# Optimization experiments

Measured on AMD Instinct MI355X. Metric: run time of the kernel, lower is better.

Reference implementation:

```python
import jax, jax.numpy as jnp
import numpy as np

B, TQ, TV, D, UNITS = 4, 256, 256, 512, 512
NEG_INF = -1e9

def setup_inputs() -> dict:
    key = jax.random.key(0)
    ks = jax.random.split(key, 5)
    return {
        "query": jax.random.normal(ks[0], (B, TQ, D), dtype=jnp.float32),
        "value": jax.random.normal(ks[1], (B, TV, D), dtype=jnp.float32),
        "mask": jnp.ones((B, TV), dtype=bool),
        "W1": jax.random.normal(ks[2], (D, UNITS), dtype=jnp.float32) * (1.0 / np.sqrt(D)),
        "W2": jax.random.normal(ks[3], (D, UNITS), dtype=jnp.float32) * (1.0 / np.sqrt(D)),
        "scale": jax.random.normal(ks[4], (UNITS,), dtype=jnp.float32),
    }

def reference(query, value, mask, W1, W2, scale):
    # Dual projections
    q = query @ W1                      # [B,Tq,U]
    k = value @ W2                      # [B,Tv,U]
    # Additive (Bahdanau) scores: sum(scale * tanh(q + k)) over units
    # broadcast tensor [B,Tq,Tv,U] is what the kernel would tile/fuse away
    t = jnp.tanh(q[:, :, None, :] + k[:, None, :, :])   # [B,Tq,Tv,U]
    scores = jnp.einsum('btvu,u->btv', t, scale)         # [B,Tq,Tv]
    # mask over value (key) positions
    scores = jnp.where(mask[:, None, :], scores, NEG_INF)
    attn = jax.nn.softmax(scores, axis=-1)               # [B,Tq,Tv]
    context = jnp.einsum('btv,bvd->btd', attn, value)    # [B,Tq,D]
    return context, attn
```

## Files before the change

### kernel.cpp

```cpp
#include <hip/hip_runtime.h>

typedef float f4 __attribute__((ext_vector_type(4)));
typedef float f2 __attribute__((ext_vector_type(2)));
typedef short short8 __attribute__((ext_vector_type(8)));
typedef float f32x4 __attribute__((ext_vector_type(4)));

#define NEG_INF -1e9f

__device__ inline void bsplit(float x, unsigned short& h, unsigned short& l) {
  union { float f; unsigned u; } a; a.f = x;
  unsigned rh = (a.u + 0x7fffu + ((a.u >> 16) & 1u)) >> 16;
  h = (unsigned short)rh;
  union { unsigned u; float f; } b; b.u = rh << 16;
  union { float f; unsigned u; } c; c.f = x - b.f;
  unsigned rl = (c.u + 0x7fffu + ((c.u >> 16) & 1u)) >> 16;
  l = (unsigned short)rl;
}

__device__ inline void gl_lds16(const void* g, void* l) {
  __builtin_amdgcn_global_load_lds(
      (const __attribute__((address_space(1))) unsigned int*)g,
      (__attribute__((address_space(3))) unsigned int*)l, 16, 0, 0);
}

__global__ __launch_bounds__(256) void conv_aw(
    const float* __restrict__ q, const float* __restrict__ v,
    const float* __restrict__ W1, const float* __restrict__ W2,
    unsigned short* __restrict__ Ahi, unsigned short* __restrict__ Alo,
    unsigned short* __restrict__ Whi, unsigned short* __restrict__ Wlo)
{
  __shared__ float ldsW[128][64];
  const int t = threadIdx.x;

  if (blockIdx.x < 512) {
    const int g = blockIdx.x * 256 + t;
    const int row64 = g & 63;
    const int panel = (g >> 6) & 31;
    const int kc    = g >> 11;
    const int rowg  = panel * 64 + row64;
    const float* src = (rowg < 1024) ? (q + (size_t)rowg * 512 + kc * 8)
                                     : (v + (size_t)(rowg - 1024) * 512 + kc * 8);
    f4 x0 = *reinterpret_cast<const f4*>(src);
    f4 x1 = *reinterpret_cast<const f4*>(src + 4);
    unsigned short h[8], l[8];
#pragma unroll
    for (int j = 0; j < 4; ++j) { bsplit(x0[j], h[j], l[j]); bsplit(x1[j], h[4+j], l[4+j]); }
    const size_t off = ((size_t)(panel * 64 + kc) * 64 + row64) * 8;
    short8 ph, pl;
#pragma unroll
    for (int j = 0; j < 8; ++j) { ph[j] = (short)h[j]; pl[j] = (short)l[j]; }
    *reinterpret_cast<short8*>(&Ahi[off]) = ph;
    *reinterpret_cast<short8*>(&Alo[off]) = pl;
    return;
  }

  const int bid   = blockIdx.x - 512;
  const int kslab = bid & 3;
  const int np    = (bid >> 2) & 7;
  const int z     = bid >> 5;
  const float* __restrict__ W = z ? W2 : W1;
  const int k0 = kslab * 128, n0 = np * 64;

#pragma unroll
  for (int it = 0; it < 8; ++it) {
    const int idx = it * 256 + t;
    const int kr  = idx >> 4;
    const int nc4 = (idx & 15) * 4;
    *reinterpret_cast<f4*>(&ldsW[kr][nc4]) =
        *reinterpret_cast<const f4*>(&W[(size_t)(k0 + kr) * 512 + n0 + nc4]);
  }
  __syncthreads();

  const int wpanel = z * 8 + np;
  const int n = t & 63;
#pragma unroll
  for (int it = 0; it < 4; ++it) {
    const int kcl = it * 4 + (t >> 6);
    short8 ph, pl;
#pragma unroll
    for (int j = 0; j < 8; ++j) {
      unsigned short h, l;
      bsplit(ldsW[kcl * 8 + j][n], h, l);
      ph[j] = (short)h; pl[j] = (short)l;
    }
    const size_t off = ((size_t)(wpanel * 64 + kslab * 16 + kcl) * 64 + n) * 8;
    *reinterpret_cast<short8*>(&Whi[off]) = ph;
    *reinterpret_cast<short8*>(&Wlo[off]) = pl;
  }
}

__global__ __launch_bounds__(256) void projmm(
    const unsigned short* __restrict__ Ahi, const unsigned short* __restrict__ Alo,
    const unsigned short* __restrict__ Whi, const unsigned short* __restrict__ Wlo,
    float* __restrict__ EQ, float* __restrict__ EKT)
{
  const int nb = blockIdx.x, mb = blockIdx.y, z = blockIdx.z;
  const int t = threadIdx.x;
  const int l = t & 63;
  const int w = t >> 6;
  const int wr = w >> 1, wc = w & 1;

  __shared__ __align__(16) short Ast[2][2][2048];
  __shared__ __align__(16) short Bst[2][2][2048];
  __shared__ float ldsT[64][67];

  const unsigned short* abase_h = Ahi + (size_t)(z * 16 + mb) * 32768;
  const unsigned short* abase_l = Alo + (size_t)(z * 16 + mb) * 32768;
  const unsigned short* wbase_h = Whi + (size_t)(z * 8 + nb) * 32768;
  const unsigned short* wbase_l = Wlo + (size_t)(z * 8 + nb) * 32768;

  const int ldst = (t >> 6) * 512;
  const int gsrc = t * 8;

#define STAGE(buf, ks)                                                        \
  do {                                                                        \
    gl_lds16(abase_h + (ks) * 2048 + gsrc, &Ast[buf][0][ldst]);               \
    gl_lds16(abase_l + (ks) * 2048 + gsrc, &Ast[buf][1][ldst]);               \
    gl_lds16(wbase_h + (ks) * 2048 + gsrc, &Bst[buf][0][ldst]);               \
    gl_lds16(wbase_l + (ks) * 2048 + gsrc, &Bst[buf][1][ldst]);               \
  } while (0)

  f32x4 acc[2][2] = {};
  STAGE(0, 0);
  __syncthreads();

  int buf = 0;
  for (int ks = 0; ks < 16; ++ks) {
    if (ks < 15) STAGE(buf ^ 1, ks + 1);
    const int kgo = (l >> 4) * 1024;
    short8 ah[2], al[2], bh[2], bl[2];
#pragma unroll
    for (int i = 0; i < 2; ++i) {
      const int ro = (wr * 32 + i * 16 + (l & 15)) * 16;
      ah[i] = *reinterpret_cast<const short8*>((const char*)&Ast[buf][0][0] + kgo + ro);
      al[i] = *reinterpret_cast<const short8*>((const char*)&Ast[buf][1][0] + kgo + ro);
    }
#pragma unroll
    for (int j = 0; j < 2; ++j) {
      const int co = (wc * 32 + j * 16 + (l & 15)) * 16;
      bh[j] = *reinterpret_cast<const short8*>((const char*)&Bst[buf][0][0] + kgo + co);
      bl[j] = *reinterpret_cast<const short8*>((const char*)&Bst[buf][1][0] + kgo + co);
    }
#pragma unroll
    for (int i = 0; i < 2; ++i)
#pragma unroll
      for (int j = 0; j < 2; ++j) {
        acc[i][j] = __builtin_amdgcn_mfma_f32_16x16x32_bf16(ah[i], bh[j], acc[i][j], 0, 0, 0);
        acc[i][j] = __builtin_amdgcn_mfma_f32_16x16x32_bf16(ah[i], bl[j], acc[i][j], 0, 0, 0);
        acc[i][j] = __builtin_amdgcn_mfma_f32_16x16x32_bf16(al[i], bh[j], acc[i][j], 0, 0, 0);
      }
    __syncthreads();
    buf ^= 1;
  }

  if (z == 0) {
#pragma unroll
    for (int i = 0; i < 2; ++i)
#pragma unroll
      for (int j = 0; j < 2; ++j)
#pragma unroll
        for (int r = 0; r < 4; ++r) {
          const int row = mb * 64 + wr * 32 + i * 16 + (l >> 4) * 4 + r;
          const int col = nb * 64 + wc * 32 + j * 16 + (l & 15);
          EQ[(size_t)row * 512 + col] = __expf(2.0f * acc[i][j][r]);
        }
  } else {
#pragma unroll
    for (int i = 0; i < 2; ++i)
#pragma unroll
      for (int j = 0; j < 2; ++j)
#pragma unroll
        for (int r = 0; r < 4; ++r) {
          const int rl = wr * 32 + i * 16 + (l >> 4) * 4 + r;
          const int cl = wc * 32 + j * 16 + (l & 15);
          ldsT[rl][cl] = __expf(2.0f * acc[i][j][r]);
        }
    __syncthreads();
    const int b  = (mb * 64) >> 8;
    const int v0 = (mb * 64) & 255;
    const int vl = t & 63;
#pragma unroll
    for (int it = 0; it < 16; ++it) {
      const int ul = it * 4 + (t >> 6);
      EKT[(size_t)b * 131072 + (size_t)(nb * 64 + ul) * 256 + v0 + vl] = ldsT[vl][ul];
    }
  }
#undef STAGE
}

__global__ __launch_bounds__(1024) void bah_attn(
    const float* __restrict__ EQ, const float* __restrict__ EKT,
    const float* __restrict__ value, const int* __restrict__ mask,
    const float* __restrict__ scale,
    float* __restrict__ ctx_out, float* __restrict__ attn_out)
{
  const int blk = blockIdx.x;
  const int b  = (blk & 7) >> 1;
  const int tg = (blk >> 3) + ((blk & 1) << 5);
  const int tq0 = tg * 4;
  const int bq  = b * 256 + tq0;

  const int tid = threadIdx.x;
  const int v4  = tid & 63;
  const int uq  = tid >> 6;
  const int w   = tid >> 6;
  const int l   = tid & 63;

  __shared__ f4    eq4s[512];
  __shared__ float ss[512];
  __shared__ float wred[4][8];
  __shared__ float sumS_lds;
  __shared__ float atT[256][4];
  __shared__ __align__(16) char uA[131072];
  float* const ubufF = (float*)uA;
  float* const partF = (float*)uA;
  float* const ctxpF = (float*)(uA + 65536);

  const float* __restrict__ ekb = EKT + (size_t)b * (512 * 256);
  const float* __restrict__ eqb = EQ + (size_t)bq * 512;

  const int u0 = uq * 32;
  float* const wbase = ubufF + uq * 2048;

#define STAGEW(bufp, s)                                                       \
  do {                                                                        \
    _Pragma("unroll")                                                         \
    for (int c_ = 0; c_ < 4; ++c_)                                            \
      gl_lds16(ekb + (size_t)(u0 + (s) * 4 + c_) * 256 + l * 4,               \
               wbase + (bufp) * 1024 + c_ * 256);                             \
  } while (0)

  STAGEW(0, 0);

  if (tid < 512) {
    f4 e;
    e[0] = eqb[tid];
    e[1] = eqb[512 + tid];
    e[2] = eqb[1024 + tid];
    e[3] = eqb[1536 + tid];
    eq4s[tid] = e;
    ss[tid] = scale[tid];
  }
  __syncthreads();

  if (w == 0) {
    float s = 0.f;
#pragma unroll
    for (int j = 0; j < 8; ++j) s += ss[l + 64 * j];
#pragma unroll
    for (int off = 32; off; off >>= 1) s += __shfl_xor(s, off);
    if (l == 0) sumS_lds = s;
  }

  f4 acc[4] = {{0,0,0,0},{0,0,0,0},{0,0,0,0},{0,0,0,0}};
  int bufi = 0;
#pragma unroll 1
  for (int s = 0; s < 8; ++s) {
    if (s < 7) {
      STAGEW(bufi ^ 1, s + 1);
      asm volatile("s_waitcnt vmcnt(4)" ::: "memory");
    } else {
      asm volatile("s_waitcnt vmcnt(0)" ::: "memory");
    }
    __builtin_amdgcn_sched_barrier(0);
    const float* bp = wbase + bufi * 1024;
#pragma unroll
    for (int cp = 0; cp < 2; ++cp) {
      const int uA_ = u0 + s * 4 + 2 * cp;
      const f4 ekA = *reinterpret_cast<const f4*>(bp + (2 * cp) * 256 + v4 * 4);
      const f4 ekB = *reinterpret_cast<const f4*>(bp + (2 * cp + 1) * 256 + v4 * 4);
      const f4 eqA = eq4s[uA_];
      const f4 eqB = eq4s[uA_ + 1];
      const float sA = ss[uA_];
      const float sB = ss[uA_ + 1];
#pragma unroll
      for (int i = 0; i < 4; ++i) {
#pragma unroll
        for (int j = 0; j < 4; ++j) {
          const float dA = fmaf(eqA[i], ekA[j], 1.0f);
          const float dB = fmaf(eqB[i], ekB[j], 1.0f);
          const float num = fmaf(sA, dB, sB * dA);
          acc[i][j] = fmaf(num, __builtin_amdgcn_rcpf(dA * dB), acc[i][j]);
        }
      }
    }
    bufi ^= 1;
  }

  __syncthreads();
#pragma unroll
  for (int i = 0; i < 4; ++i)
    *reinterpret_cast<f4*>(partF + uq * 1024 + i * 256 + v4 * 4) = acc[i];
  __syncthreads();

  float sc[4], ex[4];
  const int v = tid & 255;
  if (tid < 256) {
    const float sumS = sumS_lds;
    const bool mok = (mask[b * 256 + v] != 0);
#pragma unroll
    for (int i = 0; i < 4; ++i) {
      float p = 0.f;
#pragma unroll
      for (int u2 = 0; u2 < 16; ++u2) p += partF[u2 * 1024 + i * 256 + v];
      sc[i] = mok ? (sumS - 2.0f * p) : NEG_INF;
      float m = sc[i];
#pragma unroll
      for (int off = 32; off; off >>= 1) m = fmaxf(m, __shfl_xor(m, off));
      if (l == 0) wred[i][w] = m;
    }
  }
  __syncthreads();
  if (tid < 256) {
#pragma unroll
    for (int i = 0; i < 4; ++i) {
      const float m = fmaxf(fmaxf(wred[i][0], wred[i][1]),
                            fmaxf(wred[i][2], wred[i][3]));
      float e = __expf(sc[i] - m);
      ex[i] = e;
      float sm = e;
#pragma unroll
      for (int off = 32; off; off >>= 1) sm += __shfl_xor(sm, off);
      if (l == 0) wred[i][4 + w] = sm;
    }
  }
  __syncthreads();
  if (tid < 256) {
#pragma unroll
    for (int i = 0; i < 4; ++i) {
      const float denom = (wred[i][4] + wred[i][5]) + (wred[i][6] + wred[i][7]);
      const float a = ex[i] * __builtin_amdgcn_rcpf(denom);
      atT[v][i] = a;
      attn_out[(size_t)(bq + i) * 256 + v] = a;
    }
  }
  __syncthreads();

  const int vc = w & 3;
  const int dq = w >> 2;
  const float* __restrict__ vb = value + (size_t)b * (256 * 512);
  f2 c0v = {0.f, 0.f}, c1v = {0.f, 0.f}, c2v = {0.f, 0.f}, c3v = {0.f, 0.f};
  const int dbase = dq * 128 + l * 2;
  for (int v2 = 0; v2 < 64; ++v2) {
    const int vv = vc * 64 + v2;
    const f4 a4 = *reinterpret_cast<const f4*>(&atT[vv][0]);
    const f2 x  = *reinterpret_cast<const f2*>(&vb[(size_t)vv * 512 + dbase]);
    c0v += a4[0] * x;
    c1v += a4[1] * x;
    c2v += a4[2] * x;
    c3v += a4[3] * x;
  }
  *reinterpret_cast<f2*>(ctxpF + vc * 2048 + 0 * 512 + dbase) = c0v;
  *reinterpret_cast<f2*>(ctxpF + vc * 2048 + 1 * 512 + dbase) = c1v;
  *reinterpret_cast<f2*>(ctxpF + vc * 2048 + 2 * 512 + dbase) = c2v;
  *reinterpret_cast<f2*>(ctxpF + vc * 2048 + 3 * 512 + dbase) = c3v;
  __syncthreads();

  if (tid < 512) {
    const int i  = tid >> 7;
    const int d4 = (tid & 127) * 4;
    const f4 s0 = *reinterpret_cast<const f4*>(ctxpF + 0 * 2048 + i * 512 + d4);
    const f4 s1 = *reinterpret_cast<const f4*>(ctxpF + 1 * 2048 + i * 512 + d4);
    const f4 s2 = *reinterpret_cast<const f4*>(ctxpF + 2 * 2048 + i * 512 + d4);
    const f4 s3 = *reinterpret_cast<const f4*>(ctxpF + 3 * 2048 + i * 512 + d4);
    const f4 r = (s0 + s1) + (s2 + s3);
    *reinterpret_cast<f4*>(&ctx_out[(size_t)(bq + i) * 512 + d4]) = r;
  }
#undef STAGEW
}

extern "C" void kernel_launch(void* const* d_in, const int* in_sizes, int n_in,
                              void* d_out, int out_size, void* d_ws, size_t ws_size,
                              hipStream_t stream) {
  const float* query = (const float*)d_in[0];
  const float* value = (const float*)d_in[1];
  const int*   mask  = (const int*)d_in[2];
  const float* W1    = (const float*)d_in[3];
  const float* W2    = (const float*)d_in[4];
  const float* scale = (const float*)d_in[5];

  char* ws = (char*)d_ws;
  float* EQ  = (float*)(ws);
  float* EKT = (float*)(ws + (2u << 20));
  unsigned short* Ahi = (unsigned short*)(ws + (4u << 20));
  unsigned short* Alo = (unsigned short*)(ws + (6u << 20));
  unsigned short* Whi = (unsigned short*)(ws + (8u << 20));
  unsigned short* Wlo = (unsigned short*)(ws + (9u << 20));

  float* ctx  = (float*)d_out;
  float* attn = ctx + 4 * 256 * 512;

  conv_aw<<<dim3(576), 256, 0, stream>>>(query, value, W1, W2, Ahi, Alo, Whi, Wlo);
  projmm<<<dim3(8, 16, 2), 256, 0, stream>>>(Ahi, Alo, Whi, Wlo, EQ, EKT);
  bah_attn<<<dim3(256), 1024, 0, stream>>>(EQ, EKT, value, mask, scale, ctx, attn);
}
```

Measured before the change: 51.51 us.

## Halve query rows per block in attention kernel and double the grid

The attention kernel now handles 2 query rows per block instead of 4 and launches 512 blocks instead of 256. The unit-loop staging shrinks to 2 rows per stage over 16 stages, and LDS use drops to about half so more blocks can be resident; a min-blocks launch-bounds hint is added. The softmax now uses 512 threads, one per (row, v). The intent is to fill more CUs on the 256-CU part and shorten the per-block serial chain. The cost is that each EKT tile is read twice as often across blocks, and the value matrix is re-read by twice as many blocks.

```diff
diff --git a/kernel.cpp b/kernel.cpp
--- a/kernel.cpp
+++ b/kernel.cpp
@@ -188,7 +188,7 @@
 #undef STAGE
 }
 
-__global__ __launch_bounds__(1024) void bah_attn(
+__global__ __launch_bounds__(1024, 8) void bah_attn(
     const float* __restrict__ EQ, const float* __restrict__ EKT,
     const float* __restrict__ value, const int* __restrict__ mask,
     const float* __restrict__ scale,
@@ -196,8 +196,8 @@
 {
   const int blk = blockIdx.x;
   const int b  = (blk & 7) >> 1;
-  const int tg = (blk >> 3) + ((blk & 1) << 5);
-  const int tq0 = tg * 4;
+  const int tg = (blk >> 3) + ((blk & 1) << 6);
+  const int tq0 = tg * 2;
   const int bq  = b * 256 + tq0;
 
   const int tid = threadIdx.x;
@@ -206,39 +206,38 @@
   const int w   = tid >> 6;
   const int l   = tid & 63;
 
-  __shared__ f4    eq4s[512];
+  __shared__ f2    eq2s[512];
   __shared__ float ss[512];
-  __shared__ float wred[4][8];
+  __shared__ float wredM[2][4];
+  __shared__ float wredS[2][4];
   __shared__ float sumS_lds;
-  __shared__ float atT[256][4];
-  __shared__ __align__(16) char uA[131072];
+  __shared__ float atT[256][2];
+  __shared__ __align__(16) char uA[65536];
   float* const ubufF = (float*)uA;
   float* const partF = (float*)uA;
-  float* const ctxpF = (float*)(uA + 65536);
+  float* const ctxpF = (float*)(uA + 32768);
 
   const float* __restrict__ ekb = EKT + (size_t)b * (512 * 256);
   const float* __restrict__ eqb = EQ + (size_t)bq * 512;
 
   const int u0 = uq * 32;
-  float* const wbase = ubufF + uq * 2048;
+  float* const wbase = ubufF + uq * 1024;
 
 #define STAGEW(bufp, s)                                                       \
   do {                                                                        \
     _Pragma("unroll")                                                         \
-    for (int c_ = 0; c_ < 4; ++c_)                                            \
-      gl_lds16(ekb + (size_t)(u0 + (s) * 4 + c_) * 256 + l * 4,               \
-               wbase + (bufp) * 1024 + c_ * 256);                             \
+    for (int c_ = 0; c_ < 2; ++c_)                                            \
+      gl_lds16(ekb + (size_t)(u0 + (s) * 2 + c_) * 256 + l * 4,               \
+               wbase + (bufp) * 512 + c_ * 256);                              \
   } while (0)
 
   STAGEW(0, 0);
 
   if (tid < 512) {
-    f4 e;
+    f2 e;
     e[0] = eqb[tid];
     e[1] = eqb[512 + tid];
-    e[2] = eqb[1024 + tid];
-    e[3] = eqb[1536 + tid];
-    eq4s[tid] = e;
+    eq2s[tid] = e;
     ss[tid] = scale[tid];
   }
   __syncthreads();
@@ -252,36 +251,33 @@
     if (l == 0) sumS_lds = s;
   }
 
-  f4 acc[4] = {{0,0,0,0},{0,0,0,0},{0,0,0,0},{0,0,0,0}};
+  f4 acc[2] = {{0,0,0,0},{0,0,0,0}};
   int bufi = 0;
 #pragma unroll 1
-  for (int s = 0; s < 8; ++s) {
-    if (s < 7) {
+  for (int s = 0; s < 16; ++s) {
+    if (s < 15) {
       STAGEW(bufi ^ 1, s + 1);
-      asm volatile("s_waitcnt vmcnt(4)" ::: "memory");
+      asm volatile("s_waitcnt vmcnt(2)" ::: "memory");
     } else {
       asm volatile("s_waitcnt vmcnt(0)" ::: "memory");
     }
     __builtin_amdgcn_sched_barrier(0);
-    const float* bp = wbase + bufi * 1024;
-#pragma unroll
-    for (int cp = 0; cp < 2; ++cp) {
-      const int uA_ = u0 + s * 4 + 2 * cp;
-      const f4 ekA = *reinterpret_cast<const f4*>(bp + (2 * cp) * 256 + v4 * 4);
-      const f4 ekB = *reinterpret_cast<const f4*>(bp + (2 * cp + 1) * 256 + v4 * 4);
-      const f4 eqA = eq4s[uA_];
-      const f4 eqB = eq4s[uA_ + 1];
-      const float sA = ss[uA_];
-      const float sB = ss[uA_ + 1];
-#pragma unroll
-      for (int i = 0; i < 4; ++i) {
-#pragma unroll
-        for (int j = 0; j < 4; ++j) {
-          const float dA = fmaf(eqA[i], ekA[j], 1.0f);
-          const float dB = fmaf(eqB[i], ekB[j], 1.0f);
-          const float num = fmaf(sA, dB, sB * dA);
-          acc[i][j] = fmaf(num, __builtin_amdgcn_rcpf(dA * dB), acc[i][j]);
-        }
+    const float* bp = wbase + bufi * 512;
+    const int ua = u0 + 2 * s;
+    const f4 ekA = *reinterpret_cast<const f4*>(bp + v4 * 4);
+    const f4 ekB = *reinterpret_cast<const f4*>(bp + 256 + v4 * 4);
+    const f2 eqA = eq2s[ua];
+    const f2 eqB = eq2s[ua + 1];
+    const float sA = ss[ua];
+    const float sB = ss[ua + 1];
+#pragma unroll
+    for (int i = 0; i < 2; ++i) {
+#pragma unroll
+      for (int j = 0; j < 4; ++j) {
+        const float dA = fmaf(eqA[i], ekA[j], 1.0f);
+        const float dB = fmaf(eqB[i], ekB[j], 1.0f);
+        const float num = fmaf(sA, dB, sB * dA);
+        acc[i][j] = fmaf(num, __builtin_amdgcn_rcpf(dA * dB), acc[i][j]);
       }
     }
     bufi ^= 1;
@@ -289,82 +285,69 @@
 
   __syncthreads();
 #pragma unroll
-  for (int i = 0; i < 4; ++i)
-    *reinterpret_cast<f4*>(partF + uq * 1024 + i * 256 + v4 * 4) = acc[i];
-  __syncthreads();
-
-  float sc[4], ex[4];
-  const int v = tid & 255;
-  if (tid < 256) {
-    const float sumS = sumS_lds;
+  for (int i = 0; i < 2; ++i)
+    *reinterpret_cast<f4*>(partF + uq * 512 + i * 256 + v4 * 4) = acc[i];
+  __syncthreads();
+
+  const int r  = tid >> 8;
+  const int v  = tid & 255;
+  const int w4 = (tid >> 6) & 3;
+  float sc = 0.f, ex = 0.f;
+  if (tid < 512) {
+    float p = 0.f;
+#pragma unroll
+    for (int u2 = 0; u2 < 16; ++u2) p += partF[u2 * 512 + r * 256 + v];
     const bool mok = (mask[b * 256 + v] != 0);
-#pragma unroll
-    for (int i = 0; i < 4; ++i) {
-      float p = 0.f;
-#pragma unroll
-      for (int u2 = 0; u2 < 16; ++u2) p += partF[u2 * 1024 + i * 256 + v];
-      sc[i] = mok ? (sumS - 2.0f * p) : NEG_INF;
-      float m = sc[i];
-#pragma unroll
-      for (int off = 32; off; off >>= 1) m = fmaxf(m, __shfl_xor(m, off));
-      if (l == 0) wred[i][w] = m;
-    }
-  }
-  __syncthreads();
-  if (tid < 256) {
-#pragma unroll
-    for (int i = 0; i < 4; ++i) {
-      const float m = fmaxf(fmaxf(wred[i][0], wred[i][1]),
-                            fmaxf(wred[i][2], wred[i][3]));
-      float e = __expf(sc[i] - m);
-      ex[i] = e;
-      float sm = e;
-#pragma unroll
-      for (int off = 32; off; off >>= 1) sm += __shfl_xor(sm, off);
-      if (l == 0) wred[i][4 + w] = sm;
-    }
-  }
-  __syncthreads();
-  if (tid < 256) {
-#pragma unroll
-    for (int i = 0; i < 4; ++i) {
-      const float denom = (wred[i][4] + wred[i][5]) + (wred[i][6] + wred[i][7]);
-      const float a = ex[i] * __builtin_amdgcn_rcpf(denom);
-      atT[v][i] = a;
-      attn_out[(size_t)(bq + i) * 256 + v] = a;
-    }
+    sc = mok ? (sumS_lds - 2.0f * p) : NEG_INF;
+    float m = sc;
+#pragma unroll
+    for (int off = 32; off; off >>= 1) m = fmaxf(m, __shfl_xor(m, off));
+    if (l == 0) wredM[r][w4] = m;
+  }
+  __syncthreads();
+  if (tid < 512) {
+    const float m = fmaxf(fmaxf(wredM[r][0], wredM[r][1]),
+                          fmaxf(wredM[r][2], wredM[r][3]));
+    ex = __expf(sc - m);
+    float sm = ex;
+#pragma unroll
+    for (int off = 32; off; off >>= 1) sm += __shfl_xor(sm, off);
+    if (l == 0) wredS[r][w4] = sm;
+  }
+  __syncthreads();
+  if (tid < 512) {
+    const float denom = (wredS[r][0] + wredS[r][1]) + (wredS[r][2] + wredS[r][3]);
+    const float a = ex * __builtin_amdgcn_rcpf(denom);
+    atT[v][r] = a;
+    attn_out[(size_t)(bq + r) * 256 + v] = a;
   }
   __syncthreads();
 
   const int vc = w & 3;
   const int dq = w >> 2;
   const float* __restrict__ vb = value + (size_t)b * (256 * 512);
-  f2 c0v = {0.f, 0.f}, c1v = {0.f, 0.f}, c2v = {0.f, 0.f}, c3v = {0.f, 0.f};
+  f2 c0v = {0.f, 0.f}, c1v = {0.f, 0.f};
   const int dbase = dq * 128 + l * 2;
   for (int v2 = 0; v2 < 64; ++v2) {
     const int vv = vc * 64 + v2;
-    const f4 a4 = *reinterpret_cast<const f4*>(&atT[vv][0]);
+    const f2 a2 = *reinterpret_cast<const f2*>(&atT[vv][0]);
     const f2 x  = *reinterpret_cast<const f2*>(&vb[(size_t)vv * 512 + dbase]);
-    c0v += a4[0] * x;
-    c1v += a4[1] * x;
-    c2v += a4[2] * x;
-    c3v += a4[3] * x;
-  }
-  *reinterpret_cast<f2*>(ctxpF + vc * 2048 + 0 * 512 + dbase) = c0v;
-  *reinterpret_cast<f2*>(ctxpF + vc * 2048 + 1 * 512 + dbase) = c1v;
-  *reinterpret_cast<f2*>(ctxpF + vc * 2048 + 2 * 512 + dbase) = c2v;
-  *reinterpret_cast<f2*>(ctxpF + vc * 2048 + 3 * 512 + dbase) = c3v;
-  __syncthreads();
-
-  if (tid < 512) {
-    const int i  = tid >> 7;
-    const int d4 = (tid & 127) * 4;
-    const f4 s0 = *reinterpret_cast<const f4*>(ctxpF + 0 * 2048 + i * 512 + d4);
-    const f4 s1 = *reinterpret_cast<const f4*>(ctxpF + 1 * 2048 + i * 512 + d4);
-    const f4 s2 = *reinterpret_cast<const f4*>(ctxpF + 2 * 2048 + i * 512 + d4);
-    const f4 s3 = *reinterpret_cast<const f4*>(ctxpF + 3 * 2048 + i * 512 + d4);
-    const f4 r = (s0 + s1) + (s2 + s3);
-    *reinterpret_cast<f4*>(&ctx_out[(size_t)(bq + i) * 512 + d4]) = r;
+    c0v += a2[0] * x;
+    c1v += a2[1] * x;
+  }
+  *reinterpret_cast<f2*>(ctxpF + vc * 1024 + 0 * 512 + dbase) = c0v;
+  *reinterpret_cast<f2*>(ctxpF + vc * 1024 + 1 * 512 + dbase) = c1v;
+  __syncthreads();
+
+  if (tid < 512) {
+    const int row = tid >> 8;
+    const int d2  = (tid & 255) * 2;
+    const f2 s0 = *reinterpret_cast<const f2*>(ctxpF + 0 * 1024 + row * 512 + d2);
+    const f2 s1 = *reinterpret_cast<const f2*>(ctxpF + 1 * 1024 + row * 512 + d2);
+    const f2 s2 = *reinterpret_cast<const f2*>(ctxpF + 2 * 1024 + row * 512 + d2);
+    const f2 s3 = *reinterpret_cast<const f2*>(ctxpF + 3 * 1024 + row * 512 + d2);
+    const f2 rr = (s0 + s1) + (s2 + s3);
+    *reinterpret_cast<f2*>(&ctx_out[(size_t)(bq + row) * 512 + d2]) = rr;
   }
 #undef STAGEW
 }
@@ -392,5 +375,5 @@
 
   conv_aw<<<dim3(576), 256, 0, stream>>>(query, value, W1, W2, Ahi, Alo, Whi, Wlo);
   projmm<<<dim3(8, 16, 2), 256, 0, stream>>>(Ahi, Alo, Whi, Wlo, EQ, EKT);
-  bah_attn<<<dim3(256), 1024, 0, stream>>>(EQ, EKT, value, mask, scale, ctx, attn);
-}
+  bah_attn<<<dim3(512), 1024, 0, stream>>>(EQ, EKT, value, mask, scale, ctx, attn);
+}
```

Result: slower. 55.64 us (+8.0%).
